# Kernel tuning notes

Measured on AMD Instinct MI355X. Metric: run time of the kernel, lower is better.

Reference implementation:

```python
import jax, jax.numpy as jnp
import numpy as np

MAX_CLASSES = 10
LN_EPS = 1e-5


def _g_features(L):
    # L: (B, T, k) logits -> sorted G-matrix fingerprint (B, k*(k+1)//2)
    P = jax.nn.softmax(L, axis=-1)
    T = P.shape[1]
    k = P.shape[-1]
    G = jnp.einsum('btk,btl->bkl', P, P) / T  # (B, k, k)
    diag = jnp.diagonal(G, axis1=1, axis2=2)  # (B, k)
    diag_sorted = jnp.sort(diag, axis=-1)[:, ::-1]
    iu0, iu1 = np.triu_indices(k, 1)
    off = G[:, iu0, iu1]  # (B, k*(k-1)//2)
    off_sorted = jnp.sort(off, axis=-1)[:, ::-1]
    return jnp.concatenate([diag_sorted, off_sorted], axis=-1)


def setup_inputs() -> dict:
    key = jax.random.key(0)
    ks = list(range(2, MAX_CLASSES + 1))
    keys = jax.random.split(key, len(ks) + 3)
    B, T = 256, 4096
    inp = {}
    for i, k in enumerate(ks):
        inp[f'logits_k{k}'] = jax.random.normal(keys[i], (B, T, k), dtype=jnp.float32)
    input_dim = sum(k * (k + 1) // 2 for k in ks)  # 219
    hidden = 256
    out_dim = MAX_CLASSES - 1
    inp['ln_gamma'] = jnp.ones((input_dim,), jnp.float32)
    inp['ln_beta'] = jnp.zeros((input_dim,), jnp.float32)
    inp['w1'] = jax.random.normal(keys[-3], (input_dim, hidden), jnp.float32) * 0.05
    inp['b1'] = jnp.zeros((hidden,), jnp.float32)
    inp['w2'] = jax.random.normal(keys[-2], (hidden, hidden), jnp.float32) * 0.05
    inp['b2'] = jnp.zeros((hidden,), jnp.float32)
    inp['w3'] = jax.random.normal(keys[-1], (hidden, out_dim), jnp.float32) * 0.05
    inp['b3'] = jnp.zeros((out_dim,), jnp.float32)
    return inp


def reference(logits_k2, logits_k3, logits_k4, logits_k5, logits_k6,
              logits_k7, logits_k8, logits_k9, logits_k10,
              ln_gamma, ln_beta, w1, b1, w2, b2, w3, b3):
    all_logits = [logits_k2, logits_k3, logits_k4, logits_k5, logits_k6,
                  logits_k7, logits_k8, logits_k9, logits_k10]
    feats = jnp.concatenate([_g_features(L) for L in all_logits], axis=-1)  # (B, 219)
    # LayerNorm over last dim
    mu = jnp.mean(feats, axis=-1, keepdims=True)
    var = jnp.var(feats, axis=-1, keepdims=True)
    x = (feats - mu) * jax.lax.rsqrt(var + LN_EPS) * ln_gamma + ln_beta
    # MLP (exact GELU, matching torch nn.GELU default)
    h = jax.nn.gelu(x @ w1 + b1, approximate=False)
    h = jax.nn.gelu(h @ w2 + b2, approximate=False)
    return h @ w3 + b3  # (B, max_classes-1)
```

## Files before the change

kernel.cpp:

```cpp
#include <hip/hip_runtime.h>
#include <hip/hip_bf16.h>
#include <math.h>

#define BB 256
#define TT 4096

typedef float f4 __attribute__((ext_vector_type(4)));

__constant__ int SEGF[10] = {0, 3, 9, 19, 34, 55, 83, 119, 164, 219};

template <int K>
__device__ __forceinline__ void g_accum(const float* __restrict__ L,
                                        float* __restrict__ gdst,
                                        float* __restrict__ part, int b,
                                        int ch) {
    constexpr int NACC = K * (K + 1) / 2;
    const int tid = threadIdx.x;

    float acc[NACC];
#pragma unroll
    for (int i = 0; i < NACC; ++i) acc[i] = 0.f;

    const float* Lb = L + (size_t)b * TT * K + (size_t)ch * 2048 * K;

#pragma unroll
    for (int j = 0; j < 2; ++j) {
        const int g = tid + j * 256;
        const float* p = Lb + (size_t)g * 4 * K;
        f4 q[K];
#pragma unroll
        for (int f = 0; f < K; ++f) q[f] = *(const f4*)(p + 4 * f);

#pragma unroll
        for (int r = 0; r < 4; ++r) {
            float v[K];
#pragma unroll
            for (int c = 0; c < K; ++c) {
                const int fl = r * K + c;
                v[c] = q[fl >> 2][fl & 3];
            }
            float m = v[0];
#pragma unroll
            for (int c = 1; c < K; ++c) m = fmaxf(m, v[c]);
            float s = 0.f;
#pragma unroll
            for (int c = 0; c < K; ++c) { v[c] = __expf(v[c] - m); s += v[c]; }
            const float inv = 1.0f / s;
#pragma unroll
            for (int c = 0; c < K; ++c) v[c] *= inv;
            int idx = 0;
#pragma unroll
            for (int i = 0; i < K; ++i) {
#pragma unroll
                for (int jj = i; jj < K; ++jj) {
                    acc[idx] = fmaf(v[i], v[jj], acc[idx]);
                    ++idx;
                }
            }
        }
    }

    const int lane = tid & 63;
    const int wave = tid >> 6;
#pragma unroll
    for (int i = 0; i < NACC; ++i) {
        float x = acc[i];
#pragma unroll
        for (int off = 32; off > 0; off >>= 1) x += __shfl_down(x, off, 64);
        if (lane == 0) part[wave * 55 + i] = x;
    }
    __syncthreads();

    if (tid < NACC) {
        const float x = part[0 * 55 + tid] + part[1 * 55 + tid] +
                        part[2 * 55 + tid] + part[3 * 55 + tid];
        int i = 0, rem = tid;
        while (rem >= K - i) { rem -= K - i; ++i; }
        const int j = i + rem;
        int tgt;
        if (j == i) tgt = i;
        else tgt = K + i * (K - 1) - (i * (i - 1)) / 2 + (j - i - 1);
        gdst[tgt] = x;
    }
}

__global__ __launch_bounds__(256) void g_kernel(
    const float* __restrict__ l2, const float* __restrict__ l3,
    const float* __restrict__ l4, const float* __restrict__ l5,
    const float* __restrict__ l6, const float* __restrict__ l7,
    const float* __restrict__ l8, const float* __restrict__ l9,
    const float* __restrict__ l10, float* __restrict__ ws) {
    __shared__ float part[4 * 55];
    const int flat = blockIdx.x;
    const int kslot = flat >> 9;
    const int kidx = 8 - kslot;
    const int idx = flat & 511;
    const int b = idx >> 1;
    const int ch = idx & 1;
    float* gdst = ws + ((size_t)(b * 9 + kidx) * 2 + ch) * 55;
    switch (kidx) {
        case 0: g_accum<2>(l2, gdst, part, b, ch); break;
        case 1: g_accum<3>(l3, gdst, part, b, ch); break;
        case 2: g_accum<4>(l4, gdst, part, b, ch); break;
        case 3: g_accum<5>(l5, gdst, part, b, ch); break;
        case 4: g_accum<6>(l6, gdst, part, b, ch); break;
        case 5: g_accum<7>(l7, gdst, part, b, ch); break;
        case 6: g_accum<8>(l8, gdst, part, b, ch); break;
        case 7: g_accum<9>(l9, gdst, part, b, ch); break;
        case 8: g_accum<10>(l10, gdst, part, b, ch); break;
    }
}

__device__ __forceinline__ float gelu_exact(float x) {
    return 0.5f * x * (1.0f + erff(x * 0.70710678118654752440f));
}

__global__ __launch_bounds__(256) void head_kernel(
    const float* __restrict__ ws, const float* __restrict__ gamma,
    const float* __restrict__ beta, const float* __restrict__ w1,
    const float* __restrict__ b1, const float* __restrict__ w2,
    const float* __restrict__ b2, const float* __restrict__ w3,
    const float* __restrict__ b3, float* __restrict__ out) {
    const int b = blockIdx.x;
    const int tid = threadIdx.x;

    __shared__ float pre[219];
    __shared__ float srt[219];
    __shared__ float xln[219];
    __shared__ float h1[256];
    __shared__ float h2[256];
    __shared__ float rs1[4], rs2[4];
    __shared__ float smu, srv;

    if (tid < 219) {
        int ik = 0;
        while (tid >= SEGF[ik + 1]) ++ik;
        const int local = tid - SEGF[ik];
        const float* p0 = ws + ((size_t)(b * 9 + ik) * 2) * 55;
        pre[tid] = (p0[local] + p0[55 + local]) * (1.0f / (float)TT);
    }
    __syncthreads();

    if (tid < 219) {
        int ik = 0;
        while (tid >= SEGF[ik + 1]) ++ik;
        const int K = ik + 2;
        const int base = SEGF[ik];
        const int local = tid - base;
        int sstart, slen, lidx;
        if (local < K) { sstart = base; slen = K; lidx = local; }
        else { sstart = base + K; slen = (K * (K - 1)) / 2; lidx = local - K; }
        const float v = pre[tid];
        int rank = 0;
        for (int m = 0; m < slen; ++m) {
            const float u = pre[sstart + m];
            rank += (u > v) || ((u == v) && (m < lidx));
        }
        srt[sstart + rank] = v;
    }
    __syncthreads();

    const float val = (tid < 219) ? srt[tid] : 0.f;
    float s1 = val, s2 = val * val;
#pragma unroll
    for (int off = 32; off > 0; off >>= 1) {
        s1 += __shfl_down(s1, off, 64);
        s2 += __shfl_down(s2, off, 64);
    }
    const int wave = tid >> 6, lane = tid & 63;
    if (lane == 0) { rs1[wave] = s1; rs2[wave] = s2; }
    __syncthreads();
    if (tid == 0) {
        const float t1 = rs1[0] + rs1[1] + rs1[2] + rs1[3];
        const float t2 = rs2[0] + rs2[1] + rs2[2] + rs2[3];
        const float mu = t1 * (1.0f / 219.0f);
        const float var = t2 * (1.0f / 219.0f) - mu * mu;
        smu = mu;
        srv = rsqrtf(var + 1e-5f);
    }
    __syncthreads();
    if (tid < 219) xln[tid] = (srt[tid] - smu) * srv * gamma[tid] + beta[tid];
    __syncthreads();

    {
        float a = b1[tid];
#pragma unroll 8
        for (int i = 0; i < 219; ++i) a = fmaf(xln[i], w1[i * 256 + tid], a);
        h1[tid] = gelu_exact(a);
    }
    __syncthreads();

    {
        float c = b2[tid];
#pragma unroll 8
        for (int i = 0; i < 256; ++i) c = fmaf(h1[i], w2[i * 256 + tid], c);
        h2[tid] = gelu_exact(c);
    }
    __syncthreads();

    if (tid < 9) {
        float o = b3[tid];
#pragma unroll 8
        for (int i = 0; i < 256; ++i) o = fmaf(h2[i], w3[i * 9 + tid], o);
        out[(size_t)b * 9 + tid] = o;
    }
}

extern "C" void kernel_launch(void* const* d_in, const int* in_sizes, int n_in,
                              void* d_out, int out_size, void* d_ws,
                              size_t ws_size, hipStream_t stream) {
    const float* l2 = (const float*)d_in[0];
    const float* l3 = (const float*)d_in[1];
    const float* l4 = (const float*)d_in[2];
    const float* l5 = (const float*)d_in[3];
    const float* l6 = (const float*)d_in[4];
    const float* l7 = (const float*)d_in[5];
    const float* l8 = (const float*)d_in[6];
    const float* l9 = (const float*)d_in[7];
    const float* l10 = (const float*)d_in[8];
    const float* gamma = (const float*)d_in[9];
    const float* beta = (const float*)d_in[10];
    const float* w1 = (const float*)d_in[11];
    const float* b1 = (const float*)d_in[12];
    const float* w2 = (const float*)d_in[13];
    const float* b2 = (const float*)d_in[14];
    const float* w3 = (const float*)d_in[15];
    const float* b3 = (const float*)d_in[16];

    float* wsf = (float*)d_ws;
    float* outp = (float*)d_out;

    g_kernel<<<9 * 512, 256, 0, stream>>>(l2, l3, l4, l5, l6, l7, l8, l9, l10,
                                          wsf);
    head_kernel<<<BB, 256, 0, stream>>>(wsf, gamma, beta, w1, b1, w2, b2, w3,
                                        b3, outp);
}
```

Measured before the change: 93.50 us.

## Stage logits through padded LDS tiles with register prefetch for coalesced loads

Replaces the per-thread strided f4 loads, where each thread read 4 consecutive rows of K floats, with fully coalesced tile loads. Each tile is scattered into LDS with an odd row pitch to avoid bank conflicts, and each thread then reads one row back for the softmax and Gram accumulation. The next tile is prefetched into registers while the current one is stored, to overlap global latency with compute. This adds two barriers per tile (8 tiles) and about 11 KB of LDS per block, which may reduce occupancy and add sync overhead.

```diff
diff --git a/kernel.cpp b/kernel.cpp
--- a/kernel.cpp
+++ b/kernel.cpp
@@ -12,9 +12,13 @@
 template <int K>
 __device__ __forceinline__ void g_accum(const float* __restrict__ L,
                                         float* __restrict__ gdst,
-                                        float* __restrict__ part, int b,
-                                        int ch) {
+                                        float* __restrict__ lds,
+                                        float* __restrict__ part,
+                                        int b, int ch) {
     constexpr int NACC = K * (K + 1) / 2;
+    constexpr int PK = (K % 2 == 0) ? K + 1 : K;
+    constexpr int TILEF = 256 * K;
+    constexpr int STEPS = (K + 3) / 4;
     const int tid = threadIdx.x;
 
     float acc[NACC];
@@ -23,39 +27,58 @@
 
     const float* Lb = L + (size_t)b * TT * K + (size_t)ch * 2048 * K;
 
-#pragma unroll
-    for (int j = 0; j < 2; ++j) {
-        const int g = tid + j * 256;
-        const float* p = Lb + (size_t)g * 4 * K;
-        f4 q[K];
-#pragma unroll
-        for (int f = 0; f < K; ++f) q[f] = *(const f4*)(p + 4 * f);
-
-#pragma unroll
-        for (int r = 0; r < 4; ++r) {
-            float v[K];
-#pragma unroll
-            for (int c = 0; c < K; ++c) {
-                const int fl = r * K + c;
-                v[c] = q[fl >> 2][fl & 3];
+    f4 stage[STEPS];
+#pragma unroll
+    for (int s = 0; s < STEPS; ++s) {
+        const int fo = s * 1024 + tid * 4;
+        if (fo < TILEF) stage[s] = *(const f4*)(Lb + fo);
+    }
+
+#pragma unroll
+    for (int t = 0; t < 8; ++t) {
+        __syncthreads();
+#pragma unroll
+        for (int s = 0; s < STEPS; ++s) {
+            const int fo = s * 1024 + tid * 4;
+            if (fo < TILEF) {
+#pragma unroll
+                for (int j = 0; j < 4; ++j) {
+                    const int gl = fo + j;
+                    const int r = gl / K;
+                    const int c = gl - r * K;
+                    lds[r * PK + c] = stage[s][j];
+                }
             }
-            float m = v[0];
-#pragma unroll
-            for (int c = 1; c < K; ++c) m = fmaxf(m, v[c]);
-            float s = 0.f;
-#pragma unroll
-            for (int c = 0; c < K; ++c) { v[c] = __expf(v[c] - m); s += v[c]; }
-            const float inv = 1.0f / s;
-#pragma unroll
-            for (int c = 0; c < K; ++c) v[c] *= inv;
-            int idx = 0;
-#pragma unroll
-            for (int i = 0; i < K; ++i) {
-#pragma unroll
-                for (int jj = i; jj < K; ++jj) {
-                    acc[idx] = fmaf(v[i], v[jj], acc[idx]);
-                    ++idx;
-                }
+        }
+        if (t < 7) {
+            const float* Lt = Lb + (size_t)(t + 1) * TILEF;
+#pragma unroll
+            for (int s = 0; s < STEPS; ++s) {
+                const int fo = s * 1024 + tid * 4;
+                if (fo < TILEF) stage[s] = *(const f4*)(Lt + fo);
+            }
+        }
+        __syncthreads();
+
+        float v[K];
+#pragma unroll
+        for (int c = 0; c < K; ++c) v[c] = lds[tid * PK + c];
+        float m = v[0];
+#pragma unroll
+        for (int c = 1; c < K; ++c) m = fmaxf(m, v[c]);
+        float s = 0.f;
+#pragma unroll
+        for (int c = 0; c < K; ++c) { v[c] = __expf(v[c] - m); s += v[c]; }
+        const float inv = 1.0f / s;
+#pragma unroll
+        for (int c = 0; c < K; ++c) v[c] *= inv;
+        int idx = 0;
+#pragma unroll
+        for (int i = 0; i < K; ++i) {
+#pragma unroll
+            for (int jj = i; jj < K; ++jj) {
+                acc[idx] = fmaf(v[i], v[jj], acc[idx]);
+                ++idx;
             }
         }
     }
@@ -90,6 +113,7 @@
     const float* __restrict__ l6, const float* __restrict__ l7,
     const float* __restrict__ l8, const float* __restrict__ l9,
     const float* __restrict__ l10, float* __restrict__ ws) {
+    __shared__ float lds[256 * 11];
     __shared__ float part[4 * 55];
     const int flat = blockIdx.x;
     const int kslot = flat >> 9;
@@ -99,15 +123,15 @@
     const int ch = idx & 1;
     float* gdst = ws + ((size_t)(b * 9 + kidx) * 2 + ch) * 55;
     switch (kidx) {
-        case 0: g_accum<2>(l2, gdst, part, b, ch); break;
-        case 1: g_accum<3>(l3, gdst, part, b, ch); break;
-        case 2: g_accum<4>(l4, gdst, part, b, ch); break;
-        case 3: g_accum<5>(l5, gdst, part, b, ch); break;
-        case 4: g_accum<6>(l6, gdst, part, b, ch); break;
-        case 5: g_accum<7>(l7, gdst, part, b, ch); break;
-        case 6: g_accum<8>(l8, gdst, part, b, ch); break;
-        case 7: g_accum<9>(l9, gdst, part, b, ch); break;
-        case 8: g_accum<10>(l10, gdst, part, b, ch); break;
+        case 0: g_accum<2>(l2, gdst, lds, part, b, ch); break;
+        case 1: g_accum<3>(l3, gdst, lds, part, b, ch); break;
+        case 2: g_accum<4>(l4, gdst, lds, part, b, ch); break;
+        case 3: g_accum<5>(l5, gdst, lds, part, b, ch); break;
+        case 4: g_accum<6>(l6, gdst, lds, part, b, ch); break;
+        case 5: g_accum<7>(l7, gdst, lds, part, b, ch); break;
+        case 6: g_accum<8>(l8, gdst, lds, part, b, ch); break;
+        case 7: g_accum<9>(l9, gdst, lds, part, b, ch); break;
+        case 8: g_accum<10>(l10, gdst, lds, part, b, ch); break;
     }
 }
 
```

Result: slower. 113.0 us (+20.9%).

## Stream logits through LDS via async global_load_lds pipeline, split per-K kernels

Applied to the files above, without the earlier changes.

Replaces the monolithic switch-based G-matrix kernel with per-K templated kernels, each launched separately with 512 blocks. Each wave stages 64-row tiles of logits into a 4-slot LDS ring using global_load_lds with three tiles in flight, controlled by explicit vmcnt waits, then reads rows from LDS for softmax and outer-product accumulation. The aim is to hide global memory latency and reduce register pressure from holding wide vector loads. In exchange it adds 9 separate launches whose serialization may leave the GPU underfilled (512 blocks per launch), and it relies on hand-tuned waitcnt encodings.

```diff
diff --git a/kernel.cpp b/kernel.cpp
--- a/kernel.cpp
+++ b/kernel.cpp
@@ -7,67 +7,105 @@
 
 typedef float f4 __attribute__((ext_vector_type(4)));
 
+typedef const __attribute__((address_space(1))) void* as1_t;
+typedef __attribute__((address_space(3))) void* as3_t;
+
+__device__ __forceinline__ void gl_lds16(const float* g, const float* l) {
+    __builtin_amdgcn_global_load_lds((as1_t)g, (as3_t)l, 16, 0, 0);
+}
+
 __constant__ int SEGF[10] = {0, 3, 9, 19, 34, 55, 83, 119, 164, 219};
 
 template <int K>
-__device__ __forceinline__ void g_accum(const float* __restrict__ L,
-                                        float* __restrict__ gdst,
-                                        float* __restrict__ part, int b,
-                                        int ch) {
+__device__ __forceinline__ void row_update(float (&v)[K],
+                                           float (&acc)[K * (K + 1) / 2]) {
+    float m = v[0];
+#pragma unroll
+    for (int c = 1; c < K; ++c) m = fmaxf(m, v[c]);
+    float s = 0.f;
+#pragma unroll
+    for (int c = 0; c < K; ++c) { v[c] = __expf(v[c] - m); s += v[c]; }
+    const float inv = 1.0f / s;
+#pragma unroll
+    for (int c = 0; c < K; ++c) v[c] *= inv;
+    int idx = 0;
+#pragma unroll
+    for (int i = 0; i < K; ++i) {
+#pragma unroll
+        for (int j = i; j < K; ++j) {
+            acc[idx] = fmaf(v[i], v[j], acc[idx]);
+            ++idx;
+        }
+    }
+}
+
+template <int K>
+__global__ __launch_bounds__(256, 2) void gk(const float* __restrict__ L,
+                                             float* __restrict__ ws) {
     constexpr int NACC = K * (K + 1) / 2;
+    constexpr int VF = K / 4;
+    constexpr int RL = 16 * (K % 4);
+    constexpr int VOPS = VF + (RL ? 1 : 0);
+    constexpr int TFL = 64 * K;
+    constexpr int KIDX = K - 2;
+
+    __shared__ float lds[4 * 4 * 640 + 4 * 55];
+    float* part = lds + 4 * 4 * 640;
+
     const int tid = threadIdx.x;
+    const int lane = tid & 63;
+    const int w = tid >> 6;
+    float* buf = lds + w * 4 * 640;
+
+    const int b = blockIdx.x >> 1;
+    const int ch = blockIdx.x & 1;
+    const float* Lw =
+        L + ((size_t)b * TT + (size_t)ch * 2048 + (size_t)w * 512) * K;
 
     float acc[NACC];
 #pragma unroll
     for (int i = 0; i < NACC; ++i) acc[i] = 0.f;
 
-    const float* Lb = L + (size_t)b * TT * K + (size_t)ch * 2048 * K;
-
-#pragma unroll
-    for (int j = 0; j < 2; ++j) {
-        const int g = tid + j * 256;
-        const float* p = Lb + (size_t)g * 4 * K;
-        f4 q[K];
-#pragma unroll
-        for (int f = 0; f < K; ++f) q[f] = *(const f4*)(p + 4 * f);
-
-#pragma unroll
-        for (int r = 0; r < 4; ++r) {
-            float v[K];
-#pragma unroll
-            for (int c = 0; c < K; ++c) {
-                const int fl = r * K + c;
-                v[c] = q[fl >> 2][fl & 3];
-            }
-            float m = v[0];
-#pragma unroll
-            for (int c = 1; c < K; ++c) m = fmaxf(m, v[c]);
-            float s = 0.f;
-#pragma unroll
-            for (int c = 0; c < K; ++c) { v[c] = __expf(v[c] - m); s += v[c]; }
-            const float inv = 1.0f / s;
-#pragma unroll
-            for (int c = 0; c < K; ++c) v[c] *= inv;
-            int idx = 0;
-#pragma unroll
-            for (int i = 0; i < K; ++i) {
-#pragma unroll
-                for (int jj = i; jj < K; ++jj) {
-                    acc[idx] = fmaf(v[i], v[jj], acc[idx]);
-                    ++idx;
-                }
-            }
-        }
-    }
-
-    const int lane = tid & 63;
-    const int wave = tid >> 6;
+    auto issue = [&](int t) {
+        const float* src = Lw + (size_t)t * TFL;
+        float* dst = buf + (t & 3) * 640;
+#pragma unroll
+        for (int s = 0; s < VF; ++s)
+            gl_lds16(src + s * 256 + lane * 4, dst + s * 256);
+        if constexpr (RL > 0)
+            if (lane < RL) gl_lds16(src + VF * 256 + lane * 4, dst + VF * 256);
+    };
+
+    issue(0);
+    issue(1);
+    issue(2);
+
+#pragma unroll
+    for (int t = 0; t < 8; ++t) {
+        if (t + 3 < 8) issue(t + 3);
+        if (t < 5)
+            __builtin_amdgcn_s_waitcnt(0xF70 | (3 * VOPS));
+        else if (t == 5)
+            __builtin_amdgcn_s_waitcnt(0xF70 | (2 * VOPS));
+        else if (t == 6)
+            __builtin_amdgcn_s_waitcnt(0xF70 | (1 * VOPS));
+        else
+            __builtin_amdgcn_s_waitcnt(0xF70);
+        __builtin_amdgcn_sched_barrier(0);
+
+        const float* myrow = buf + (t & 3) * 640 + lane * K;
+        float v[K];
+#pragma unroll
+        for (int c = 0; c < K; ++c) v[c] = myrow[c];
+        row_update<K>(v, acc);
+    }
+
 #pragma unroll
     for (int i = 0; i < NACC; ++i) {
         float x = acc[i];
 #pragma unroll
         for (int off = 32; off > 0; off >>= 1) x += __shfl_down(x, off, 64);
-        if (lane == 0) part[wave * 55 + i] = x;
+        if (lane == 0) part[w * 55 + i] = x;
     }
     __syncthreads();
 
@@ -80,34 +118,8 @@
         int tgt;
         if (j == i) tgt = i;
         else tgt = K + i * (K - 1) - (i * (i - 1)) / 2 + (j - i - 1);
+        float* gdst = ws + ((size_t)(b * 9 + KIDX) * 2 + ch) * 55;
         gdst[tgt] = x;
-    }
-}
-
-__global__ __launch_bounds__(256) void g_kernel(
-    const float* __restrict__ l2, const float* __restrict__ l3,
-    const float* __restrict__ l4, const float* __restrict__ l5,
-    const float* __restrict__ l6, const float* __restrict__ l7,
-    const float* __restrict__ l8, const float* __restrict__ l9,
-    const float* __restrict__ l10, float* __restrict__ ws) {
-    __shared__ float part[4 * 55];
-    const int flat = blockIdx.x;
-    const int kslot = flat >> 9;
-    const int kidx = 8 - kslot;
-    const int idx = flat & 511;
-    const int b = idx >> 1;
-    const int ch = idx & 1;
-    float* gdst = ws + ((size_t)(b * 9 + kidx) * 2 + ch) * 55;
-    switch (kidx) {
-        case 0: g_accum<2>(l2, gdst, part, b, ch); break;
-        case 1: g_accum<3>(l3, gdst, part, b, ch); break;
-        case 2: g_accum<4>(l4, gdst, part, b, ch); break;
-        case 3: g_accum<5>(l5, gdst, part, b, ch); break;
-        case 4: g_accum<6>(l6, gdst, part, b, ch); break;
-        case 5: g_accum<7>(l7, gdst, part, b, ch); break;
-        case 6: g_accum<8>(l8, gdst, part, b, ch); break;
-        case 7: g_accum<9>(l9, gdst, part, b, ch); break;
-        case 8: g_accum<10>(l10, gdst, part, b, ch); break;
     }
 }
 
@@ -230,8 +242,15 @@
     float* wsf = (float*)d_ws;
     float* outp = (float*)d_out;
 
-    g_kernel<<<9 * 512, 256, 0, stream>>>(l2, l3, l4, l5, l6, l7, l8, l9, l10,
-                                          wsf);
+    gk<10><<<512, 256, 0, stream>>>(l10, wsf);
+    gk<9><<<512, 256, 0, stream>>>(l9, wsf);
+    gk<8><<<512, 256, 0, stream>>>(l8, wsf);
+    gk<7><<<512, 256, 0, stream>>>(l7, wsf);
+    gk<6><<<512, 256, 0, stream>>>(l6, wsf);
+    gk<5><<<512, 256, 0, stream>>>(l5, wsf);
+    gk<4><<<512, 256, 0, stream>>>(l4, wsf);
+    gk<3><<<512, 256, 0, stream>>>(l3, wsf);
+    gk<2><<<512, 256, 0, stream>>>(l2, wsf);
     head_kernel<<<BB, 256, 0, stream>>>(wsf, gamma, beta, w1, b1, w2, b2, w3,
                                         b3, outp);
 }
```

Result: slower. 158.4 us (+69.4%).
